# Kernel optimization log

Measured on AMD Instinct MI355X. Metric: run time of the kernel, lower is better.

## Reference

```python
import jax, jax.numpy as jnp
import numpy as np
import math

H = 16
D_ATTN = 64
D_MID = 64
D_X = 1024
D_Z = 1024
D_OUT = 1024
B = 2
L_X = 2048
L_Z = 2048
MINUS_INFINITY = -1000000.0

def _xavier(key, shape):
    fan_in, fan_out = shape
    limit = math.sqrt(6.0 / (fan_in + fan_out))
    return jax.random.uniform(key, shape, jnp.float32, -limit, limit)

def setup_inputs() -> dict:
    key = jax.random.key(0)
    ks = jax.random.split(key, 8)
    primary = jax.random.normal(ks[0], (B, L_X, D_X), jnp.float32)
    context = jax.random.normal(ks[1], (B, L_Z, D_Z), jnp.float32)
    padding_mask = jnp.ones((B, L_Z), jnp.int32)
    # causal attention mask (b, l_x, l_z)
    attention_mask = jnp.broadcast_to(
        jnp.tril(jnp.ones((L_X, L_Z), jnp.int32))[None], (B, L_X, L_Z))
    W_qs = _xavier(ks[2], (D_X, H * D_ATTN))
    W_ks = _xavier(ks[3], (D_Z, H * D_ATTN))
    W_vs = _xavier(ks[4], (D_Z, H * D_MID))
    W_o = _xavier(ks[5], (H * D_MID, D_OUT))
    b_o = jnp.zeros((D_OUT,), jnp.float32)
    return {"primary": primary, "context": context,
            "padding_mask": padding_mask, "attention_mask": attention_mask,
            "W_qs": W_qs, "W_ks": W_ks, "W_vs": W_vs, "W_o": W_o, "b_o": b_o}

def reference(primary, context, padding_mask, attention_mask, W_qs, W_ks, W_vs, W_o, b_o):
    b, l_x, _ = primary.shape
    l_z = context.shape[1]
    # QKV projections, split into heads (head-major columns)
    q = (primary @ W_qs).reshape(b, l_x, H, D_ATTN).transpose(0, 2, 1, 3)  # (b,h,l_x,d_attn)
    k = (context @ W_ks).reshape(b, l_z, H, D_ATTN).transpose(0, 2, 1, 3)  # (b,h,l_z,d_attn)
    v = (context @ W_vs).reshape(b, l_z, H, D_MID).transpose(0, 2, 1, 3)   # (b,h,l_z,d_mid)
    scores = jnp.einsum('bhxd,bhzd->bhxz', q, k) / math.sqrt(D_ATTN)
    # combined mask: attention_mask AND padding_mask, broadcast over heads
    mask = (attention_mask * padding_mask[:, None, :])[:, None]  # (b,1,l_x,l_z)
    scores = jnp.where(mask == 0, MINUS_INFINITY, scores)
    attn = jax.nn.softmax(scores, axis=-1)
    out = jnp.einsum('bhxz,bhzm->bhxm', attn, v)  # (b,h,l_x,d_mid)
    out = out.transpose(0, 2, 1, 3).reshape(b, l_x, H * D_MID)
    return out @ W_o + b_o
```

## Files before the change

### kernel.cpp

```cpp
#include <hip/hip_runtime.h>

#define NB 2
#define LX 2048
#define LZ 2048
#define HH 16
#define DA 64
#define DM 64
#define HD 1024
#define MINF  -1000000.0f
#define QSC   0.1803368801f
#define DTHR  8.0f

typedef __attribute__((ext_vector_type(8))) short short8;
typedef __attribute__((ext_vector_type(4))) float f32x4;

static __device__ __forceinline__ ushort f2bf(float f) {
    union { float f; uint32_t u; } c; c.f = f;
    return (ushort)((c.u + 0x7FFFu + ((c.u >> 16) & 1u)) >> 16);
}

static __device__ __forceinline__ uint32_t cvtpk(float lo, float hi) {
    uint32_t r;
    asm("v_cvt_pk_bf16_f32 %0, %1, %2" : "=v"(r) : "v"(lo), "v"(hi));
    return r;
}

#define GL16(g, l) __builtin_amdgcn_global_load_lds( \
    (const __attribute__((address_space(1))) void*)(g), \
    (__attribute__((address_space(3))) void*)(l), 16, 0, 0)

__global__ __launch_bounds__(256) void cvt_both(
    const float* __restrict__ pA, const float* __restrict__ pB,
    ushort* __restrict__ oA, ushort* __restrict__ oB)
{
    const int i = blockIdx.x * 256 + threadIdx.x;
    const float* in = (i < 1048576) ? pA : pB;
    ushort* out = (i < 1048576) ? oA : oB;
    const int j = i & 1048575;
    float4 v = ((const float4*)in)[j];
    ushort4 o;
    o.x = f2bf(v.x); o.y = f2bf(v.y); o.z = f2bf(v.z); o.w = f2bf(v.w);
    ((ushort4*)out)[j] = o;
}

__global__ __launch_bounds__(256) void wtrans4(
    const float* __restrict__ W0, const float* __restrict__ W1,
    const float* __restrict__ W2, const float* __restrict__ W3,
    ushort* __restrict__ T0, ushort* __restrict__ T1,
    ushort* __restrict__ T2, ushort* __restrict__ T3)
{
    const int zz = blockIdx.z;
    const float* W = (zz == 0) ? W0 : (zz == 1) ? W1 : (zz == 2) ? W2 : W3;
    ushort* Wt = (zz == 0) ? T0 : (zz == 1) ? T1 : (zz == 2) ? T2 : T3;

    __shared__ ushort Ls[64][72];
    const int n0 = blockIdx.x * 64, k0 = blockIdx.y * 64;
    const int t = threadIdx.x;
    const int rr = t >> 4, c4 = (t & 15) * 4;
    #pragma unroll
    for (int i = 0; i < 4; ++i) {
        const int r = rr + i * 16;
        float4 v = *(const float4*)&W[(size_t)(k0 + r) * 1024 + n0 + c4];
        Ls[c4 + 0][r] = f2bf(v.x);
        Ls[c4 + 1][r] = f2bf(v.y);
        Ls[c4 + 2][r] = f2bf(v.z);
        Ls[c4 + 3][r] = f2bf(v.w);
    }
    __syncthreads();
    const int n = t >> 2, kc = (t & 3) * 16;
    *(short8*)&Wt[(size_t)(n0 + n) * 1024 + k0 + kc]     = *(const short8*)&Ls[n][kc];
    *(short8*)&Wt[(size_t)(n0 + n) * 1024 + k0 + kc + 8] = *(const short8*)&Ls[n][kc + 8];
}

template <bool OUTF32>
static __device__ __forceinline__ void gemm_body(
    const ushort* __restrict__ A, const ushort* __restrict__ Bt,
    const float* __restrict__ bias, void* __restrict__ Cout, float osc)
{
    __shared__ ushort As[128 * 32];
    __shared__ ushort Bs[128 * 32];
    const int t = threadIdx.x;
    const int w = t >> 6, l = t & 63, lr = l & 15, lg = l >> 4;
    const int wr = w >> 1, wc = w & 1;
    const int n0 = blockIdx.x * 128, m0 = blockIdx.y * 128;

    const int c0 = t, c1 = t + 256;
    const ushort* a0 = &A[(size_t)(m0 + (c0 >> 2)) * 1024 + (c0 & 3) * 8];
    const ushort* a1 = &A[(size_t)(m0 + (c1 >> 2)) * 1024 + (c1 & 3) * 8];
    const ushort* b0 = &Bt[(size_t)(n0 + (c0 >> 2)) * 1024 + (c0 & 3) * 8];
    const ushort* b1 = &Bt[(size_t)(n0 + (c1 >> 2)) * 1024 + (c1 & 3) * 8];
    ushort* lA0 = &As[w * 512];
    ushort* lA1 = &As[(4 + w) * 512];
    ushort* lB0 = &Bs[w * 512];
    ushort* lB1 = &Bs[(4 + w) * 512];

    f32x4 acc[4][4];
    #pragma unroll
    for (int i = 0; i < 4; ++i)
        #pragma unroll
        for (int j = 0; j < 4; ++j) acc[i][j] = 0.f;

    for (int k0 = 0; k0 < 1024; k0 += 32) {
        __syncthreads();
        GL16(a0 + k0, lA0);
        GL16(a1 + k0, lA1);
        GL16(b0 + k0, lB0);
        GL16(b1 + k0, lB1);
        __syncthreads();
        short8 af[4], bf[4];
        #pragma unroll
        for (int mi = 0; mi < 4; ++mi)
            af[mi] = *(const short8*)&As[(wr * 64 + mi * 16 + lr) * 32 + lg * 8];
        #pragma unroll
        for (int nj = 0; nj < 4; ++nj)
            bf[nj] = *(const short8*)&Bs[(wc * 64 + nj * 16 + lr) * 32 + lg * 8];
        #pragma unroll
        for (int mi = 0; mi < 4; ++mi)
            #pragma unroll
            for (int nj = 0; nj < 4; ++nj)
                acc[mi][nj] = __builtin_amdgcn_mfma_f32_16x16x32_bf16(
                    af[mi], bf[nj], acc[mi][nj], 0, 0, 0);
    }

    const int row0 = m0 + wr * 64, col0 = n0 + wc * 64;
    #pragma unroll
    for (int mi = 0; mi < 4; ++mi)
        #pragma unroll
        for (int nj = 0; nj < 4; ++nj) {
            const int col = col0 + nj * 16 + lr;
            #pragma unroll
            for (int r = 0; r < 4; ++r) {
                const int row = row0 + mi * 16 + lg * 4 + r;
                const float v = acc[mi][nj][r];
                if (OUTF32)
                    ((float*)Cout)[(size_t)row * 1024 + col] = v + bias[col];
                else
                    ((ushort*)Cout)[(size_t)row * 1024 + col] = f2bf(v * osc);
            }
        }
}

__global__ __launch_bounds__(256) void gemm_qkv(
    const ushort* __restrict__ Pb, const ushort* __restrict__ Cb,
    const ushort* __restrict__ Wqt, const ushort* __restrict__ Wkt,
    const ushort* __restrict__ Wvt,
    ushort* __restrict__ Qb, ushort* __restrict__ Kb, ushort* __restrict__ Vb)
{
    const int z = blockIdx.z;
    const ushort* A  = (z == 0) ? Pb : Cb;
    const ushort* Bt = (z == 0) ? Wqt : (z == 1) ? Wkt : Wvt;
    ushort* C = (z == 0) ? Qb : (z == 1) ? Kb : Vb;
    const float osc = (z == 0) ? QSC : 1.0f;
    gemm_body<false>(A, Bt, nullptr, C, osc);
}

__global__ __launch_bounds__(256) void gemm_out(
    const ushort* __restrict__ A, const ushort* __restrict__ Bt,
    const float* __restrict__ bias, float* __restrict__ Cout)
{
    gemm_body<true>(A, Bt, bias, Cout, 1.0f);
}

__global__ __launch_bounds__(256) void mask_classify(
    const int* __restrict__ amask, const int* __restrict__ pmask,
    int* __restrict__ cls)
{
    const int bid = blockIdx.x;
    const int b = bid >> 10, xb = (bid >> 5) & 31, zb = bid & 31;
    const int t = threadIdx.x;
    int andv = 1, orv = 0;
    #pragma unroll
    for (int i = 0; i < 16; ++i) {
        const int e = t + i * 256;
        const int r = e >> 6, z = e & 63;
        const int m = amask[((size_t)b * LX + xb * 64 + r) * LZ + zb * 64 + z];
        const int p = pmask[(size_t)b * LZ + zb * 64 + z];
        const int v = (m != 0) & (p != 0);
        andv &= v; orv |= v;
    }
    __shared__ int sa[256];
    __shared__ int so[256];
    sa[t] = andv; so[t] = orv;
    __syncthreads();
    for (int s = 128; s > 0; s >>= 1) {
        if (t < s) { sa[t] &= sa[t + s]; so[t] |= so[t + s]; }
        __syncthreads();
    }
    if (t == 0) cls[bid] = so[0] ? (sa[0] ? 1 : 2) : 0;
}

__global__ __launch_bounds__(256, 4) void attn_mfma(
    const ushort* __restrict__ Qg, const ushort* __restrict__ Kg,
    const ushort* __restrict__ Vg, const int* __restrict__ amask,
    const int* __restrict__ pmask, const int* __restrict__ cls,
    ushort* __restrict__ O)
{
    __shared__ ushort Ks[64 * 72];
    __shared__ ushort Vt[64 * 64];

    const int t = threadIdx.x, w = t >> 6, l = t & 63, lr = l & 15, lg = l >> 4;
    const int x = blockIdx.x, h = blockIdx.y, b = blockIdx.z;
    const int fx = (x & 1) ? 31 - (x >> 1) : (x >> 1);
    const int qb = b ? 31 - fx : fx;
    const int qw = qb * 64 + w * 16;

    short8 qf[2];
    #pragma unroll
    for (int ks = 0; ks < 2; ++ks)
        qf[ks] = *(const short8*)&Qg[(size_t)(b * LX + qw + lr) * HD
                                     + h * DA + ks * 32 + lg * 8];

    float mrun = -1e30f, lrun = 0.f;
    f32x4 o[4];
    #pragma unroll
    for (int mj = 0; mj < 4; ++mj) o[mj] = 0.f;

    const int kz = t >> 2, kc = (t & 3) * 16;
    const int vz = (t >> 3) * 2, vc = (t & 7) * 8;

    for (int zb = 0; zb < LZ / 64; ++zb) {
        const int cl = cls[b * 1024 + qb * 32 + zb];
        if (cl == 0) continue;
        const int z0 = zb * 64;

        __syncthreads();
        {
            const ushort* kp = &Kg[(size_t)(b * LZ + z0 + kz) * HD + h * DA + kc];
            *(short8*)&Ks[kz * 72 + kc]     = *(const short8*)kp;
            *(short8*)&Ks[kz * 72 + kc + 8] = *(const short8*)(kp + 8);
            const ushort* vp = &Vg[(size_t)(b * LZ + z0 + vz) * HD + h * DM + vc];
            short8 v0 = *(const short8*)vp;
            short8 v1 = *(const short8*)(vp + HD);
            const int zc = vz >> 3, zo = vz & 7;
            #pragma unroll
            for (int j = 0; j < 8; ++j) {
                const int m = vc + j;
                const int idx = m * 64 + (((zc ^ m ^ (m >> 3)) & 7) << 3) + zo;
                const uint32_t pr = (uint32_t)(ushort)v0[j] | ((uint32_t)(ushort)v1[j] << 16);
                *(uint32_t*)&Vt[idx] = pr;
            }
        }
        __syncthreads();

        f32x4 s[4];
        __builtin_amdgcn_s_setprio(1);
        #pragma unroll
        for (int nj = 0; nj < 4; ++nj) {
            const short8 kf0 = *(const short8*)&Ks[(nj * 16 + lr) * 72 + lg * 8];
            const short8 kf1 = *(const short8*)&Ks[(nj * 16 + lr) * 72 + 32 + lg * 8];
            f32x4 z4 = 0.f;
            z4 = __builtin_amdgcn_mfma_f32_16x16x32_bf16(kf0, qf[0], z4, 0, 0, 0);
            z4 = __builtin_amdgcn_mfma_f32_16x16x32_bf16(kf1, qf[1], z4, 0, 0, 0);
            s[nj] = z4;
        }
        __builtin_amdgcn_s_setprio(0);
        if (cl == 2) {
            const size_t arow = (size_t)(b * LX + qw + lr) * LZ + z0;
            #pragma unroll
            for (int nj = 0; nj < 4; ++nj)
                #pragma unroll
                for (int r = 0; r < 4; ++r) {
                    const int z = nj * 16 + lg * 4 + r;
                    const int ok = (amask[arow + z] != 0) & (pmask[b * LZ + z0 + z] != 0);
                    if (!ok) s[nj][r] = MINF;
                }
        }
        {
            float pm = s[0][0];
            #pragma unroll
            for (int nj = 0; nj < 4; ++nj)
                #pragma unroll
                for (int r = 0; r < 4; ++r) pm = fmaxf(pm, s[nj][r]);
            pm = fmaxf(pm, __shfl_xor(pm, 16));
            pm = fmaxf(pm, __shfl_xor(pm, 32));
            if (__any(pm > mrun + DTHR)) {
                const float mn = fmaxf(mrun, pm);
                const float al = exp2f(mrun - mn);
                mrun = mn;
                lrun *= al;
                #pragma unroll
                for (int r = 0; r < 4; ++r) {
                    const float alq = __shfl(al, (lg << 2) + r);
                    #pragma unroll
                    for (int mj = 0; mj < 4; ++mj) o[mj][r] *= alq;
                }
            }
            float sum = 0.f;
            #pragma unroll
            for (int nj = 0; nj < 4; ++nj)
                #pragma unroll
                for (int r = 0; r < 4; ++r) {
                    const float p = exp2f(s[nj][r] - mrun);
                    s[nj][r] = p;
                    sum += p;
                }
            sum += __shfl_xor(sum, 16);
            sum += __shfl_xor(sum, 32);
            lrun += sum;
        }
        short8 pa[2];
        {
            uint32_t pk01[4], pk23[4];
            #pragma unroll
            for (int nj = 0; nj < 4; ++nj) {
                pk01[nj] = cvtpk(s[nj][0], s[nj][1]);
                pk23[nj] = cvtpk(s[nj][2], s[nj][3]);
            }
            #pragma unroll
            for (int ks = 0; ks < 2; ++ks) {
                union { uint32_t d[4]; short8 v; } u;
                u.d[0] = pk01[2 * ks];
                u.d[1] = pk23[2 * ks];
                u.d[2] = pk01[2 * ks + 1];
                u.d[3] = pk23[2 * ks + 1];
                pa[ks] = u.v;
            }
        }
        __builtin_amdgcn_s_setprio(1);
        #pragma unroll
        for (int mj = 0; mj < 4; ++mj) {
            const int m_ = mj * 16 + lr;
            const int xr = (m_ ^ (m_ >> 3)) & 7;
            const int czb = lg >> 1;
            const int zo = (lg & 1) * 4;
            #pragma unroll
            for (int ks = 0; ks < 2; ++ks) {
                const int clo = (ks * 4 + czb) ^ xr;
                const int chi = (ks * 4 + 2 + czb) ^ xr;
                const uint2 lo = *(const uint2*)&Vt[m_ * 64 + ((clo & 7) << 3) + zo];
                const uint2 hi = *(const uint2*)&Vt[m_ * 64 + ((chi & 7) << 3) + zo];
                union { uint32_t d[4]; short8 v; } u;
                u.d[0] = lo.x; u.d[1] = lo.y; u.d[2] = hi.x; u.d[3] = hi.y;
                o[mj] = __builtin_amdgcn_mfma_f32_16x16x32_bf16(pa[ks], u.v, o[mj], 0, 0, 0);
            }
        }
        __builtin_amdgcn_s_setprio(0);
    }

    const float linv = 1.f / lrun;
    #pragma unroll
    for (int r = 0; r < 4; ++r) {
        const float iq = __shfl(linv, (lg << 2) + r);
        #pragma unroll
        for (int mj = 0; mj < 4; ++mj)
            O[(size_t)(b * LX + qw + (lg << 2) + r) * HD + h * DM + mj * 16 + lr]
                = f2bf(o[mj][r] * iq);
    }
}

extern "C" void kernel_launch(void* const* d_in, const int* in_sizes, int n_in,
                              void* d_out, int out_size, void* d_ws, size_t ws_size,
                              hipStream_t stream)
{
    const float* primary = (const float*)d_in[0];
    const float* context = (const float*)d_in[1];
    const int*   pmask   = (const int*)d_in[2];
    const int*   amask   = (const int*)d_in[3];
    const float* Wq      = (const float*)d_in[4];
    const float* Wk      = (const float*)d_in[5];
    const float* Wv      = (const float*)d_in[6];
    const float* Wo      = (const float*)d_in[7];
    const float* bo      = (const float*)d_in[8];
    float* out = (float*)d_out;

    char* w8 = (char*)d_ws;
    ushort* Pb  = (ushort*)(w8 + 0);
    ushort* Cb  = (ushort*)(w8 + 8388608);
    ushort* Qb  = (ushort*)(w8 + 16777216);
    ushort* Kb  = (ushort*)(w8 + 25165824);
    ushort* Vb  = (ushort*)(w8 + 33554432);
    ushort* AOb = (ushort*)(w8 + 41943040);
    ushort* Wqt = (ushort*)(w8 + 50331648);
    ushort* Wkt = (ushort*)(w8 + 52428800);
    ushort* Wvt = (ushort*)(w8 + 54525952);
    ushort* Wot = (ushort*)(w8 + 56623104);
    int*    clsp = (int*)(w8 + 58720256);

    cvt_both<<<8192, 256, 0, stream>>>(primary, context, Pb, Cb);
    wtrans4<<<dim3(16, 16, 4), 256, 0, stream>>>(Wq, Wk, Wv, Wo, Wqt, Wkt, Wvt, Wot);
    mask_classify<<<NB * 32 * 32, 256, 0, stream>>>(amask, pmask, clsp);
    gemm_qkv<<<dim3(8, 32, 3), 256, 0, stream>>>(Pb, Cb, Wqt, Wkt, Wvt, Qb, Kb, Vb);
    attn_mfma<<<dim3(32, 16, 2), 256, 0, stream>>>(Qb, Kb, Vb, amask, pmask, clsp, AOb);
    gemm_out<<<dim3(8, 32), 256, 0, stream>>>(AOb, Wot, bo, out);
}
```

Before: 139.0 us.

## Split attention KV range across two blocks and merge partials in combine kernel

Each attention block now processes only every other KV tile, doubling the grid to improve occupancy and load balance for the causal workload. Each split writes unnormalized bf16 partial outputs plus per-row max and sum, and a new combine kernel rescales and merges the two halves. The per-iteration cross-lane sum reduction is deferred to the end, and launch bounds are raised to 8 waves per EU. Costs are an extra kernel launch, extra global traffic for the partials, and bf16 rounding of unnormalized partials.

```diff
diff --git a/kernel.cpp b/kernel.cpp
--- a/kernel.cpp
+++ b/kernel.cpp
@@ -17,6 +17,11 @@
 static __device__ __forceinline__ ushort f2bf(float f) {
     union { float f; uint32_t u; } c; c.f = f;
     return (ushort)((c.u + 0x7FFFu + ((c.u >> 16) & 1u)) >> 16);
+}
+
+static __device__ __forceinline__ float bf2f(ushort u) {
+    union { uint32_t u; float f; } c; c.u = (uint32_t)u << 16;
+    return c.f;
 }
 
 static __device__ __forceinline__ uint32_t cvtpk(float lo, float hi) {
@@ -189,17 +194,18 @@
     if (t == 0) cls[bid] = so[0] ? (sa[0] ? 1 : 2) : 0;
 }
 
-__global__ __launch_bounds__(256, 4) void attn_mfma(
+__global__ __launch_bounds__(256, 8) void attn_mfma(
     const ushort* __restrict__ Qg, const ushort* __restrict__ Kg,
     const ushort* __restrict__ Vg, const int* __restrict__ amask,
     const int* __restrict__ pmask, const int* __restrict__ cls,
-    ushort* __restrict__ O)
+    ushort* __restrict__ Op, float2* __restrict__ ml)
 {
     __shared__ ushort Ks[64 * 72];
     __shared__ ushort Vt[64 * 64];
 
     const int t = threadIdx.x, w = t >> 6, l = t & 63, lr = l & 15, lg = l >> 4;
-    const int x = blockIdx.x, h = blockIdx.y, b = blockIdx.z;
+    const int x = blockIdx.x, h = blockIdx.y;
+    const int b = blockIdx.z >> 1, sKV = blockIdx.z & 1;
     const int fx = (x & 1) ? 31 - (x >> 1) : (x >> 1);
     const int qb = b ? 31 - fx : fx;
     const int qw = qb * 64 + w * 16;
@@ -218,7 +224,7 @@
     const int kz = t >> 2, kc = (t & 3) * 16;
     const int vz = (t >> 3) * 2, vc = (t & 7) * 8;
 
-    for (int zb = 0; zb < LZ / 64; ++zb) {
+    for (int zb = sKV; zb < LZ / 64; zb += 2) {
         const int cl = cls[b * 1024 + qb * 32 + zb];
         if (cl == 0) continue;
         const int z0 = zb * 64;
@@ -285,18 +291,14 @@
                     for (int mj = 0; mj < 4; ++mj) o[mj][r] *= alq;
                 }
             }
-            float sum = 0.f;
             #pragma unroll
             for (int nj = 0; nj < 4; ++nj)
                 #pragma unroll
                 for (int r = 0; r < 4; ++r) {
                     const float p = exp2f(s[nj][r] - mrun);
                     s[nj][r] = p;
-                    sum += p;
+                    lrun += p;
                 }
-            sum += __shfl_xor(sum, 16);
-            sum += __shfl_xor(sum, 32);
-            lrun += sum;
         }
         short8 pa[2];
         {
@@ -337,15 +339,42 @@
         __builtin_amdgcn_s_setprio(0);
     }
 
-    const float linv = 1.f / lrun;
-    #pragma unroll
-    for (int r = 0; r < 4; ++r) {
-        const float iq = __shfl(linv, (lg << 2) + r);
+    lrun += __shfl_xor(lrun, 16);
+    lrun += __shfl_xor(lrun, 32);
+    if (l < 16)
+        ml[(size_t)((sKV * NB + b) * HH + h) * LX + qw + l] = make_float2(mrun, lrun);
+    const size_t ob = (size_t)((sKV * NB + b) * LX + qw) * HD + h * DM;
+    #pragma unroll
+    for (int r = 0; r < 4; ++r)
         #pragma unroll
         for (int mj = 0; mj < 4; ++mj)
-            O[(size_t)(b * LX + qw + (lg << 2) + r) * HD + h * DM + mj * 16 + lr]
-                = f2bf(o[mj][r] * iq);
-    }
+            Op[ob + (size_t)((lg << 2) + r) * HD + mj * 16 + lr] = f2bf(o[mj][r]);
+}
+
+__global__ __launch_bounds__(256) void attn_combine(
+    const ushort* __restrict__ Op, const float2* __restrict__ ml,
+    ushort* __restrict__ AOb)
+{
+    const int gid = blockIdx.x * 256 + threadIdx.x;
+    if (gid >= NB * LX * HD / 8) return;
+    const int row = gid >> 7;
+    const int b = row >> 11, xx = row & 2047;
+    const int h = (gid >> 3) & 15;
+    const size_t e0 = (size_t)row * HD + (size_t)(gid & 127) * 8;
+    const short8 p0 = *(const short8*)&Op[e0];
+    const short8 p1 = *(const short8*)&Op[(size_t)NB * LX * HD + e0];
+    const int mi = (b * HH + h) * LX + xx;
+    const float2 a0 = ml[mi];
+    const float2 a1 = ml[NB * HH * LX + mi];
+    const float M = fmaxf(a0.x, a1.x);
+    float w0 = exp2f(a0.x - M), w1 = exp2f(a1.x - M);
+    const float inv = 1.f / (a0.y * w0 + a1.y * w1);
+    w0 *= inv; w1 *= inv;
+    short8 o;
+    #pragma unroll
+    for (int j = 0; j < 8; ++j)
+        o[j] = (short)f2bf(bf2f((ushort)p0[j]) * w0 + bf2f((ushort)p1[j]) * w1);
+    *(short8*)&AOb[e0] = o;
 }
 
 extern "C" void kernel_launch(void* const* d_in, const int* in_sizes, int n_in,
@@ -375,11 +404,14 @@
     ushort* Wvt = (ushort*)(w8 + 54525952);
     ushort* Wot = (ushort*)(w8 + 56623104);
     int*    clsp = (int*)(w8 + 58720256);
+    ushort* Op  = Pb;
+    float2* mlp = (float2*)Wqt;
 
     cvt_both<<<8192, 256, 0, stream>>>(primary, context, Pb, Cb);
     wtrans4<<<dim3(16, 16, 4), 256, 0, stream>>>(Wq, Wk, Wv, Wo, Wqt, Wkt, Wvt, Wot);
     mask_classify<<<NB * 32 * 32, 256, 0, stream>>>(amask, pmask, clsp);
     gemm_qkv<<<dim3(8, 32, 3), 256, 0, stream>>>(Pb, Cb, Wqt, Wkt, Wvt, Qb, Kb, Vb);
-    attn_mfma<<<dim3(32, 16, 2), 256, 0, stream>>>(Qb, Kb, Vb, amask, pmask, clsp, AOb);
+    attn_mfma<<<dim3(32, 16, 4), 256, 0, stream>>>(Qb, Kb, Vb, amask, pmask, clsp, Op, mlp);
+    attn_combine<<<2048, 256, 0, stream>>>(Op, mlp, AOb);
     gemm_out<<<dim3(8, 32), 256, 0, stream>>>(AOb, Wot, bo, out);
 }
```

New measurement: 231.6 us. +66.6%, slower.

## Double-buffer K/V tiles with register prefetch and XCD-aware block remap

Applied to the files above, without the earlier changes.

Adds double-buffered LDS for K and V, prefetching the next active tile into registers while the current one is computed. This removes one barrier per iteration and hides global load latency. Active and mixed tiles are found up front with a ballot over the class array, so the loop visits only non-empty tiles. Block indices are remapped so blocks sharing a head and batch land on the same XCD for L2 reuse. The row-sum shuffle reduction is deferred to the end, and a fully masked query block writes zeros and exits early.

```diff
diff --git a/kernel.cpp b/kernel.cpp
--- a/kernel.cpp
+++ b/kernel.cpp
@@ -195,14 +195,32 @@
     const int* __restrict__ pmask, const int* __restrict__ cls,
     ushort* __restrict__ O)
 {
-    __shared__ ushort Ks[64 * 72];
-    __shared__ ushort Vt[64 * 64];
+    __shared__ ushort Ks[2][64 * 72];
+    __shared__ ushort Vt[2][64 * 64];
 
     const int t = threadIdx.x, w = t >> 6, l = t & 63, lr = l & 15, lg = l >> 4;
-    const int x = blockIdx.x, h = blockIdx.y, b = blockIdx.z;
-    const int fx = (x & 1) ? 31 - (x >> 1) : (x >> 1);
+    const int flat = blockIdx.x + 32 * (blockIdx.y + 16 * blockIdx.z);
+    const int xcd = flat & 7, ii = flat >> 3;
+    const int g = xcd + 8 * (ii >> 5);
+    const int xr_ = ii & 31;
+    const int h = g & 15, b = g >> 4;
+    const int fx = (xr_ & 1) ? 31 - (xr_ >> 1) : (xr_ >> 1);
     const int qb = b ? 31 - fx : fx;
     const int qw = qb * 64 + w * 16;
+
+    const int cv = cls[b * 1024 + qb * 32 + (l & 31)];
+    const uint32_t act = (uint32_t)__ballot(cv != 0);
+    const uint32_t mix = (uint32_t)__ballot(cv == 2);
+
+    const size_t obase = (size_t)(b * LX + qw) * HD + h * DM;
+    if (act == 0) {
+        #pragma unroll
+        for (int r = 0; r < 4; ++r)
+            #pragma unroll
+            for (int mj = 0; mj < 4; ++mj)
+                O[obase + (size_t)((lg << 2) + r) * HD + mj * 16 + lr] = 0;
+        return;
+    }
 
     short8 qf[2];
     #pragma unroll
@@ -218,43 +236,61 @@
     const int kz = t >> 2, kc = (t & 3) * 16;
     const int vz = (t >> 3) * 2, vc = (t & 7) * 8;
 
-    for (int zb = 0; zb < LZ / 64; ++zb) {
-        const int cl = cls[b * 1024 + qb * 32 + zb];
-        if (cl == 0) continue;
+    short8 kr0, kr1, vr0, vr1;
+
+#define PREFETCH(zbx) do {                                                     \
+        const int z0p = (zbx) * 64;                                           \
+        const ushort* kp = &Kg[(size_t)(b * LZ + z0p + kz) * HD + h * DA + kc];\
+        kr0 = *(const short8*)kp;                                             \
+        kr1 = *(const short8*)(kp + 8);                                       \
+        const ushort* vp = &Vg[(size_t)(b * LZ + z0p + vz) * HD + h * DM + vc];\
+        vr0 = *(const short8*)vp;                                             \
+        vr1 = *(const short8*)(vp + HD);                                      \
+    } while (0)
+
+#define WRITE_LDS(bi) do {                                                     \
+        *(short8*)&Ks[bi][kz * 72 + kc]     = kr0;                            \
+        *(short8*)&Ks[bi][kz * 72 + kc + 8] = kr1;                            \
+        const int zc = vz >> 3, zo = vz & 7;                                  \
+        _Pragma("unroll")                                                      \
+        for (int j = 0; j < 8; ++j) {                                         \
+            const int m = vc + j;                                             \
+            const int idx = m * 64 + (((zc ^ m ^ (m >> 3)) & 7) << 3) + zo;   \
+            *(uint32_t*)&Vt[bi][idx] =                                        \
+                (uint32_t)(ushort)vr0[j] | ((uint32_t)(ushort)vr1[j] << 16);  \
+        }                                                                      \
+    } while (0)
+
+    int zb = __builtin_ctz(act);
+    uint32_t rem = act & (act - 1);
+    PREFETCH(zb);
+    WRITE_LDS(0);
+    __syncthreads();
+    int cur = 0;
+
+    for (;;) {
+        const bool mixed = (mix >> zb) & 1;
         const int z0 = zb * 64;
-
-        __syncthreads();
-        {
-            const ushort* kp = &Kg[(size_t)(b * LZ + z0 + kz) * HD + h * DA + kc];
-            *(short8*)&Ks[kz * 72 + kc]     = *(const short8*)kp;
-            *(short8*)&Ks[kz * 72 + kc + 8] = *(const short8*)(kp + 8);
-            const ushort* vp = &Vg[(size_t)(b * LZ + z0 + vz) * HD + h * DM + vc];
-            short8 v0 = *(const short8*)vp;
-            short8 v1 = *(const short8*)(vp + HD);
-            const int zc = vz >> 3, zo = vz & 7;
-            #pragma unroll
-            for (int j = 0; j < 8; ++j) {
-                const int m = vc + j;
-                const int idx = m * 64 + (((zc ^ m ^ (m >> 3)) & 7) << 3) + zo;
-                const uint32_t pr = (uint32_t)(ushort)v0[j] | ((uint32_t)(ushort)v1[j] << 16);
-                *(uint32_t*)&Vt[idx] = pr;
-            }
-        }
-        __syncthreads();
+        int zbn = -1;
+        if (rem) {
+            zbn = __builtin_ctz(rem);
+            rem &= rem - 1;
+            PREFETCH(zbn);
+        }
 
         f32x4 s[4];
         __builtin_amdgcn_s_setprio(1);
         #pragma unroll
         for (int nj = 0; nj < 4; ++nj) {
-            const short8 kf0 = *(const short8*)&Ks[(nj * 16 + lr) * 72 + lg * 8];
-            const short8 kf1 = *(const short8*)&Ks[(nj * 16 + lr) * 72 + 32 + lg * 8];
+            const short8 kf0 = *(const short8*)&Ks[cur][(nj * 16 + lr) * 72 + lg * 8];
+            const short8 kf1 = *(const short8*)&Ks[cur][(nj * 16 + lr) * 72 + 32 + lg * 8];
             f32x4 z4 = 0.f;
             z4 = __builtin_amdgcn_mfma_f32_16x16x32_bf16(kf0, qf[0], z4, 0, 0, 0);
             z4 = __builtin_amdgcn_mfma_f32_16x16x32_bf16(kf1, qf[1], z4, 0, 0, 0);
             s[nj] = z4;
         }
         __builtin_amdgcn_s_setprio(0);
-        if (cl == 2) {
+        if (mixed) {
             const size_t arow = (size_t)(b * LX + qw + lr) * LZ + z0;
             #pragma unroll
             for (int nj = 0; nj < 4; ++nj)
@@ -285,18 +321,14 @@
                     for (int mj = 0; mj < 4; ++mj) o[mj][r] *= alq;
                 }
             }
-            float sum = 0.f;
             #pragma unroll
             for (int nj = 0; nj < 4; ++nj)
                 #pragma unroll
                 for (int r = 0; r < 4; ++r) {
                     const float p = exp2f(s[nj][r] - mrun);
                     s[nj][r] = p;
-                    sum += p;
+                    lrun += p;
                 }
-            sum += __shfl_xor(sum, 16);
-            sum += __shfl_xor(sum, 32);
-            lrun += sum;
         }
         short8 pa[2];
         {
@@ -327,25 +359,35 @@
             for (int ks = 0; ks < 2; ++ks) {
                 const int clo = (ks * 4 + czb) ^ xr;
                 const int chi = (ks * 4 + 2 + czb) ^ xr;
-                const uint2 lo = *(const uint2*)&Vt[m_ * 64 + ((clo & 7) << 3) + zo];
-                const uint2 hi = *(const uint2*)&Vt[m_ * 64 + ((chi & 7) << 3) + zo];
+                const uint2 lo = *(const uint2*)&Vt[cur][m_ * 64 + ((clo & 7) << 3) + zo];
+                const uint2 hi = *(const uint2*)&Vt[cur][m_ * 64 + ((chi & 7) << 3) + zo];
                 union { uint32_t d[4]; short8 v; } u;
                 u.d[0] = lo.x; u.d[1] = lo.y; u.d[2] = hi.x; u.d[3] = hi.y;
                 o[mj] = __builtin_amdgcn_mfma_f32_16x16x32_bf16(pa[ks], u.v, o[mj], 0, 0, 0);
             }
         }
         __builtin_amdgcn_s_setprio(0);
-    }
-
+
+        if (zbn < 0) break;
+        WRITE_LDS(cur ^ 1);
+        __syncthreads();
+        cur ^= 1;
+        zb = zbn;
+    }
+
+    lrun += __shfl_xor(lrun, 16);
+    lrun += __shfl_xor(lrun, 32);
     const float linv = 1.f / lrun;
     #pragma unroll
     for (int r = 0; r < 4; ++r) {
         const float iq = __shfl(linv, (lg << 2) + r);
         #pragma unroll
         for (int mj = 0; mj < 4; ++mj)
-            O[(size_t)(b * LX + qw + (lg << 2) + r) * HD + h * DM + mj * 16 + lr]
+            O[obase + (size_t)((lg << 2) + r) * HD + mj * 16 + lr]
                 = f2bf(o[mj][r] * iq);
     }
+#undef PREFETCH
+#undef WRITE_LDS
 }
 
 extern "C" void kernel_launch(void* const* d_in, const int* in_sizes, int n_in,
```

Result: slower. 142.0 us (+2.1%).
